# Optimization experiments

Measured on AMD Instinct MI355X. Metric: run time of the kernel, lower is better.

Reference implementation:

```python
import jax, jax.numpy as jnp
import numpy as np

BLOCK = 128          # per-block quantization group size (BLOCK_SIZE in source)
FP8_MAX = 448.0      # max representable magnitude of float8_e4m3fn


def _quantize(x2d):
    # Per-128-element block quantization along the last (contiguous) dim,
    # matching quantize_fp8_triton applied to the row-major flattened tensor.
    R, K = x2d.shape
    xb = x2d.reshape(R, K // BLOCK, BLOCK)
    s = jnp.max(jnp.abs(xb), axis=-1) / FP8_MAX            # [R, K//BLOCK] fp32 scales
    y = (xb / s[..., None]).astype(jnp.float8_e4m3fn)      # fp8 payload
    return y, s


def _dequantize(y, s):
    # Inline dequant: fp8 -> fp32 times per-block scale (fused into GEMM accum in the kernel).
    return (y.astype(jnp.float32) * s[..., None]).reshape(y.shape[0], -1)


def setup_inputs() -> dict:
    key = jax.random.key(0)
    kx, kw = jax.random.split(key)
    B, T, D, O = 4, 2048, 4096, 4096
    x = jax.random.normal(kx, (B, T, D), dtype=jnp.float32)
    limit = float(np.sqrt(6.0 / (D + O)))  # xavier_uniform_
    weight = jax.random.uniform(kw, (O, D), minval=-limit, maxval=limit, dtype=jnp.float32)
    return {"x": x, "weight": weight}


def reference(x, weight):
    B, T, D = x.shape
    xf = x.reshape(-1, D)                  # [M, K]
    xq, xs = _quantize(xf)                 # fp8 activations + per-(row,kblock) scales
    wq, ws = _quantize(weight)             # fp8 weights + per-(row,kblock) scales
    # Block-scaled GEMM: sum_i (A_i @ B_i^T) * a_s[:, i] * b_s[:, i]
    # expressed equivalently as dequant-then-matmul (identical math, fp32 accumulate).
    out = _dequantize(xq, xs) @ _dequantize(wq, ws).T      # [M, N]
    return out.reshape(B, T, -1)
```

## Files before the change

### kernel.cpp

```cpp
#include <hip/hip_runtime.h>

using u16 = unsigned short;
typedef int i32x4 __attribute__((ext_vector_type(4)));
typedef int i32x8 __attribute__((ext_vector_type(8)));
typedef float f32x4 __attribute__((ext_vector_type(4)));
typedef float f32x2 __attribute__((ext_vector_type(2)));
typedef float f32x16 __attribute__((ext_vector_type(16)));

#define SC1 0x7F7F7F7F

__device__ inline void async16(const void* g, void* l) {
    __builtin_amdgcn_global_load_lds(
        (__attribute__((address_space(1))) void*)(g),
        (__attribute__((address_space(3))) void*)(l),
        16, 0, 0);
}

__device__ inline i32x8 mk8(i32x4 lo, i32x4 hi) {
    return __builtin_shufflevector(lo, hi, 0, 1, 2, 3, 4, 5, 6, 7);
}

__global__ void quant_kernel(const float* __restrict__ in,
                             u16* __restrict__ outq,
                             float* __restrict__ outs,
                             long R) {
    long wid = (long)blockIdx.x * 4 + (threadIdx.x >> 6);
    int lane = threadIdx.x & 63;
    if (wid >= R * 32) return;

    float2 v = reinterpret_cast<const float2*>(in + wid * 128)[lane];
    float a = fmaxf(fabsf(v.x), fabsf(v.y));
#pragma unroll
    for (int off = 32; off; off >>= 1) a = fmaxf(a, __shfl_xor(a, off));

    float s = a / 448.0f;
    float qx = v.x / s;
    float qy = v.y / s;
    qx = fminf(fmaxf(qx, -448.0f), 448.0f);
    qy = fminf(fmaxf(qy, -448.0f), 448.0f);

    int pk = __builtin_amdgcn_cvt_pk_fp8_f32(qx, qy, 0, false);
    outq[wid * 64 + lane] = (u16)(pk & 0xFFFF);

    if (lane == 0) {
        long row = wid >> 5, kb = wid & 31;
        outs[kb * R + row] = s;
    }
}


#define SWZ(x) ((x) ^ ((((x) >> 7) & 7) << 4))

__global__ __launch_bounds__(512, 2) void gemm_fp8(
    const char* __restrict__ Aq, const char* __restrict__ Bq,
    const float* __restrict__ AscaleG, const float* __restrict__ BscaleG,
    float* __restrict__ C, int M, int N) {
    extern __shared__ __align__(16) char smem[];
    const int KB = 4096;

    const int tid = threadIdx.x;
    const int wid = tid >> 6;
    const int lane = tid & 63;
    const int l31 = lane & 31;
    const int lh = lane >> 5;
    const int wr = wid >> 2;
    const int wc = wid & 3;

    int nwg = gridDim.x, bid = blockIdx.x, swz = bid;
    if ((nwg & 7) == 0) swz = (bid & 7) * (nwg >> 3) + (bid >> 3);
    const int nbn = N >> 8;
    const long brow = (long)(swz / nbn) << 8;
    const long bcol = (long)(swz % nbn) << 8;

    const char* Abase = Aq + brow * KB;
    const char* Bbase = Bq + bcol * KB;

    int aofs[4];
#pragma unroll
    for (int c = 0; c < 4; ++c) {
        int dloc = c * 8192 + wid * 1024 + lane * 16;
        int l = SWZ(dloc);
        aofs[c] = (l >> 7) * KB + (l & 127);
    }

    int cox[4];
#pragma unroll
    for (int kh = 0; kh < 2; ++kh)
#pragma unroll
        for (int hh = 0; hh < 2; ++hh)
            cox[kh * 2 + hh] = (((kh << 6) | (lh << 5) | (hh << 4)) ^ ((lane & 7) << 4));

    int arowb[4], brown[2];
#pragma unroll
    for (int b = 0; b < 4; ++b) arowb[b] = (wr * 128 + b * 32 + l31) << 7;
#pragma unroll
    for (int n = 0; n < 2; ++n) brown[n] = (wc * 64 + n * 32 + l31) << 7;

#define STAGE(kb_, bufb) { \
    _Pragma("unroll") for (int c_ = 0; c_ < 4; ++c_) { \
        char* dA_ = smem + (bufb) * 32768 + c_ * 8192 + wid * 1024; \
        char* dB_ = dA_ + 65536; \
        async16(Abase + aofs[c_] + (kb_) * 128, dA_); \
        async16(Bbase + aofs[c_] + (kb_) * 128, dB_); } \
    if (wid == 0) \
        async16((const char*)AscaleG + ((long)(kb_) * M + brow) * 4 + lane * 16, \
                smem + 131072 + (bufb) * 1024); \
    if (wid == 1) \
        async16((const char*)BscaleG + ((long)(kb_) * N + bcol) * 4 + lane * 16, \
                smem + 133120 + (bufb) * 1024); }

    f32x16 acc[4][2];
#pragma unroll
    for (int b = 0; b < 4; ++b)
#pragma unroll
        for (int n = 0; n < 2; ++n)
#pragma unroll
            for (int e = 0; e < 16; ++e) acc[b][n][e] = 0.f;

    STAGE(0, 0);
    asm volatile("s_waitcnt vmcnt(0)" ::: "memory");
    __builtin_amdgcn_s_barrier();

    for (int kb = 0; kb < 32; ++kb) {
        const int buf = kb & 1;
        if (kb < 31) STAGE(kb + 1, buf ^ 1);

        const char* Ab = smem + buf * 32768;
        const char* Bb = Ab + 65536;
        const float* SaB = (const float*)(smem + 131072 + buf * 1024);
        const float* SbB = (const float*)(smem + 133120 + buf * 1024);

        i32x8 b8[2][2];
#pragma unroll
        for (int n = 0; n < 2; ++n)
#pragma unroll
            for (int kh = 0; kh < 2; ++kh)
                b8[n][kh] = mk8(*(const i32x4*)(Bb + brown[n] + cox[kh * 2]),
                                *(const i32x4*)(Bb + brown[n] + cox[kh * 2 + 1]));
        float sbv[2];
#pragma unroll
        for (int n = 0; n < 2; ++n) sbv[n] = SbB[wc * 64 + n * 32 + l31];

        __builtin_amdgcn_s_setprio(1);
#pragma unroll
        for (int b = 0; b < 4; ++b) {
            i32x8 a0 = mk8(*(const i32x4*)(Ab + arowb[b] + cox[0]),
                           *(const i32x4*)(Ab + arowb[b] + cox[1]));
            i32x8 a1 = mk8(*(const i32x4*)(Ab + arowb[b] + cox[2]),
                           *(const i32x4*)(Ab + arowb[b] + cox[3]));
            f32x4 sa4[4];
#pragma unroll
            for (int i = 0; i < 4; ++i)
                sa4[i] = *(const f32x4*)(SaB + wr * 128 + b * 32 + 4 * lh + 8 * i);
#pragma unroll
            for (int n = 0; n < 2; ++n) {
                f32x16 t = __builtin_amdgcn_mfma_scale_f32_32x32x64_f8f6f4(
                    a0, b8[n][0], (f32x16)(0.f), 0, 0, 0, SC1, 0, SC1);
                t = __builtin_amdgcn_mfma_scale_f32_32x32x64_f8f6f4(
                    a1, b8[n][1], t, 0, 0, 0, SC1, 0, SC1);
#pragma unroll
                for (int e = 0; e < 16; ++e)
                    acc[b][n][e] = fmaf(t[e], sa4[e >> 2][e & 3] * sbv[n],
                                        acc[b][n][e]);
            }
        }
        __builtin_amdgcn_s_setprio(0);

        asm volatile("s_waitcnt vmcnt(0)" ::: "memory");
        __builtin_amdgcn_s_barrier();
    }

#pragma unroll
    for (int b = 0; b < 4; ++b)
#pragma unroll
        for (int n = 0; n < 2; ++n)
#pragma unroll
            for (int e = 0; e < 16; ++e) {
                long r = brow + wr * 128 + b * 32 + (e & 3) + 8 * (e >> 2) + 4 * lh;
                long cc = bcol + wc * 64 + n * 32 + l31;
                C[r * (long)N + cc] = acc[b][n][e];
            }
#undef STAGE
}

extern "C" void kernel_launch(void* const* d_in, const int* in_sizes, int n_in,
                              void* d_out, int out_size, void* d_ws, size_t ws_size,
                              hipStream_t stream) {
    const float* x = (const float*)d_in[0];
    const float* w = (const float*)d_in[1];
    float* out = (float*)d_out;

    const int K = 4096;
    const long M = (long)in_sizes[0] / K;
    const long N = (long)in_sizes[1] / K;

    u16* Aq = (u16*)d_ws;
    u16* Bq = Aq + (size_t)M * K / 2;
    float* Asc = (float*)(Bq + (size_t)N * K / 2);
    float* Bsc = Asc + 32 * (size_t)M;

    const long nblkA = M * 32, nblkB = N * 32;
    quant_kernel<<<dim3((unsigned)((nblkA + 3) / 4)), dim3(256), 0, stream>>>(
        x, Aq, Asc, M);
    quant_kernel<<<dim3((unsigned)((nblkB + 3) / 4)), dim3(256), 0, stream>>>(
        w, Bq, Bsc, N);

    static int smem_set = 0;
    if (!smem_set) {
        hipFuncSetAttribute((const void*)gemm_fp8,
                            hipFuncAttributeMaxDynamicSharedMemorySize, 135168);
        smem_set = 1;
    }
    dim3 grid((unsigned)((M / 256) * (N / 256)));
    gemm_fp8<<<grid, dim3(512), 135168, stream>>>(
        (const char*)Aq, (const char*)Bq, Asc, Bsc, out, (int)M, (int)N);
}
```

Measured before the change: 289.7 us.

## Software-pipeline FP8 GEMM main loop with register double-buffered A bands

Restructures the K loop of the block-scaled FP8 GEMM into four phases per K block. The next A band is read from LDS while the current band runs MFMAs, and the global-to-LDS copies for the next K block are split across the phases. Scale loads are now issued by every wave instead of only waves 0 and 1, and the final K block is peeled off. The aim is to hide LDS read latency and spread global load issue more evenly across compute, at the cost of more barriers per iteration, redundant scale traffic and more register pressure.

Result: slower. 642.6 us (+121.8%).

```diff
diff --git a/kernel.cpp b/kernel.cpp
--- a/kernel.cpp
+++ b/kernel.cpp
@@ -51,12 +51,16 @@
 
 #define SWZ(x) ((x) ^ ((((x) >> 7) & 7) << 4))
 
+#define FENCE asm volatile("" ::: "memory");
+#define BARRIER { __builtin_amdgcn_s_barrier(); FENCE }
+#define VMC0 { asm volatile("s_waitcnt vmcnt(0)" ::: "memory"); }
+
 __global__ __launch_bounds__(512, 2) void gemm_fp8(
     const char* __restrict__ Aq, const char* __restrict__ Bq,
     const float* __restrict__ AscaleG, const float* __restrict__ BscaleG,
     float* __restrict__ C, int M, int N) {
     extern __shared__ __align__(16) char smem[];
-    const int KB = 4096;
+    const int KBYTES = 4096;
 
     const int tid = threadIdx.x;
     const int wid = tid >> 6;
@@ -72,15 +76,15 @@
     const long brow = (long)(swz / nbn) << 8;
     const long bcol = (long)(swz % nbn) << 8;
 
-    const char* Abase = Aq + brow * KB;
-    const char* Bbase = Bq + bcol * KB;
+    const char* Abase = Aq + brow * KBYTES;
+    const char* Bbase = Bq + bcol * KBYTES;
 
     int aofs[4];
 #pragma unroll
     for (int c = 0; c < 4; ++c) {
         int dloc = c * 8192 + wid * 1024 + lane * 16;
         int l = SWZ(dloc);
-        aofs[c] = (l >> 7) * KB + (l & 127);
+        aofs[c] = (l >> 7) * KBYTES + (l & 127);
     }
 
     int cox[4];
@@ -88,7 +92,8 @@
     for (int kh = 0; kh < 2; ++kh)
 #pragma unroll
         for (int hh = 0; hh < 2; ++hh)
-            cox[kh * 2 + hh] = (((kh << 6) | (lh << 5) | (hh << 4)) ^ ((lane & 7) << 4));
+            cox[kh * 2 + hh] =
+                (((kh << 6) | (lh << 5) | (hh << 4)) ^ ((lane & 7) << 4));
 
     int arowb[4], brown[2];
 #pragma unroll
@@ -96,18 +101,54 @@
 #pragma unroll
     for (int n = 0; n < 2; ++n) brown[n] = (wc * 64 + n * 32 + l31) << 7;
 
-#define STAGE(kb_, bufb) { \
-    _Pragma("unroll") for (int c_ = 0; c_ < 4; ++c_) { \
-        char* dA_ = smem + (bufb) * 32768 + c_ * 8192 + wid * 1024; \
-        char* dB_ = dA_ + 65536; \
-        async16(Abase + aofs[c_] + (kb_) * 128, dA_); \
-        async16(Bbase + aofs[c_] + (kb_) * 128, dB_); } \
-    if (wid == 0) \
-        async16((const char*)AscaleG + ((long)(kb_) * M + brow) * 4 + lane * 16, \
-                smem + 131072 + (bufb) * 1024); \
-    if (wid == 1) \
-        async16((const char*)BscaleG + ((long)(kb_) * N + bcol) * 4 + lane * 16, \
-                smem + 133120 + (bufb) * 1024); }
+#define STG_SCALES(kb1) { \
+    async16((const char*)AscaleG + ((long)(kb1) * M + brow) * 4 + lane * 16, \
+            smem + 131072 + ((kb1) & 1) * 1024); \
+    async16((const char*)BscaleG + ((long)(kb1) * N + bcol) * 4 + lane * 16, \
+            smem + 133120 + ((kb1) & 1) * 1024); }
+
+#define STG_DATA(kb1, c_) { \
+    char* dA_ = smem + ((kb1) & 1) * 32768 + (c_) * 8192 + wid * 1024; \
+    async16(Abase + aofs[c_] + (long)(kb1) * 128, dA_); \
+    async16(Bbase + aofs[c_] + (long)(kb1) * 128, dA_ + 65536); }
+
+#define RD_HEAD(bufb) { \
+    const char* Bb_ = smem + 65536 + (bufb) * 32768; \
+    _Pragma("unroll") for (int n_ = 0; n_ < 2; ++n_) \
+    _Pragma("unroll") for (int kh_ = 0; kh_ < 2; ++kh_) \
+        b8[n_][kh_] = mk8(*(const i32x4*)(Bb_ + brown[n_] + cox[kh_ * 2]), \
+                          *(const i32x4*)(Bb_ + brown[n_] + cox[kh_ * 2 + 1])); \
+    const float* Sb_ = (const float*)(smem + 133120 + (bufb) * 1024); \
+    sbv0 = Sb_[wc * 64 + l31]; \
+    sbv1 = Sb_[wc * 64 + 32 + l31]; }
+
+#define RD_BAND(b_, bufb, A0, A1, SA) { \
+    const char* Ab_ = smem + (bufb) * 32768; \
+    A0 = mk8(*(const i32x4*)(Ab_ + arowb[b_] + cox[0]), \
+             *(const i32x4*)(Ab_ + arowb[b_] + cox[1])); \
+    A1 = mk8(*(const i32x4*)(Ab_ + arowb[b_] + cox[2]), \
+             *(const i32x4*)(Ab_ + arowb[b_] + cox[3])); \
+    const float* Sa_ = (const float*)(smem + 131072 + (bufb) * 1024); \
+    _Pragma("unroll") for (int i_ = 0; i_ < 4; ++i_) \
+        SA[i_] = *(const f32x4*)(Sa_ + wr * 128 + (b_) * 32 + 4 * lh + 8 * i_); }
+
+#define COMPUTE(b_, A0, A1, SA) { \
+    __builtin_amdgcn_s_setprio(1); \
+    f32x16 t0_ = __builtin_amdgcn_mfma_scale_f32_32x32x64_f8f6f4( \
+        A0, b8[0][0], (f32x16)(0.f), 0, 0, 0, SC1, 0, SC1); \
+    t0_ = __builtin_amdgcn_mfma_scale_f32_32x32x64_f8f6f4( \
+        A1, b8[0][1], t0_, 0, 0, 0, SC1, 0, SC1); \
+    f32x16 t1_ = __builtin_amdgcn_mfma_scale_f32_32x32x64_f8f6f4( \
+        A0, b8[1][0], (f32x16)(0.f), 0, 0, 0, SC1, 0, SC1); \
+    t1_ = __builtin_amdgcn_mfma_scale_f32_32x32x64_f8f6f4( \
+        A1, b8[1][1], t1_, 0, 0, 0, SC1, 0, SC1); \
+    __builtin_amdgcn_s_setprio(0); \
+    _Pragma("unroll") for (int i_ = 0; i_ < 4; ++i_) \
+    _Pragma("unroll") for (int j_ = 0; j_ < 4; ++j_) { \
+        acc[b_][0][i_ * 4 + j_] = fmaf(t0_[i_ * 4 + j_], SA[i_][j_] * sbv0, \
+                                       acc[b_][0][i_ * 4 + j_]); \
+        acc[b_][1][i_ * 4 + j_] = fmaf(t1_[i_ * 4 + j_], SA[i_][j_] * sbv1, \
+                                       acc[b_][1][i_ * 4 + j_]); } }
 
     f32x16 acc[4][2];
 #pragma unroll
@@ -117,57 +158,45 @@
 #pragma unroll
             for (int e = 0; e < 16; ++e) acc[b][n][e] = 0.f;
 
-    STAGE(0, 0);
-    asm volatile("s_waitcnt vmcnt(0)" ::: "memory");
-    __builtin_amdgcn_s_barrier();
-
-    for (int kb = 0; kb < 32; ++kb) {
-        const int buf = kb & 1;
-        if (kb < 31) STAGE(kb + 1, buf ^ 1);
-
-        const char* Ab = smem + buf * 32768;
-        const char* Bb = Ab + 65536;
-        const float* SaB = (const float*)(smem + 131072 + buf * 1024);
-        const float* SbB = (const float*)(smem + 133120 + buf * 1024);
-
-        i32x8 b8[2][2];
-#pragma unroll
-        for (int n = 0; n < 2; ++n)
-#pragma unroll
-            for (int kh = 0; kh < 2; ++kh)
-                b8[n][kh] = mk8(*(const i32x4*)(Bb + brown[n] + cox[kh * 2]),
-                                *(const i32x4*)(Bb + brown[n] + cox[kh * 2 + 1]));
-        float sbv[2];
-#pragma unroll
-        for (int n = 0; n < 2; ++n) sbv[n] = SbB[wc * 64 + n * 32 + l31];
-
-        __builtin_amdgcn_s_setprio(1);
-#pragma unroll
-        for (int b = 0; b < 4; ++b) {
-            i32x8 a0 = mk8(*(const i32x4*)(Ab + arowb[b] + cox[0]),
-                           *(const i32x4*)(Ab + arowb[b] + cox[1]));
-            i32x8 a1 = mk8(*(const i32x4*)(Ab + arowb[b] + cox[2]),
-                           *(const i32x4*)(Ab + arowb[b] + cox[3]));
-            f32x4 sa4[4];
-#pragma unroll
-            for (int i = 0; i < 4; ++i)
-                sa4[i] = *(const f32x4*)(SaB + wr * 128 + b * 32 + 4 * lh + 8 * i);
-#pragma unroll
-            for (int n = 0; n < 2; ++n) {
-                f32x16 t = __builtin_amdgcn_mfma_scale_f32_32x32x64_f8f6f4(
-                    a0, b8[n][0], (f32x16)(0.f), 0, 0, 0, SC1, 0, SC1);
-                t = __builtin_amdgcn_mfma_scale_f32_32x32x64_f8f6f4(
-                    a1, b8[n][1], t, 0, 0, 0, SC1, 0, SC1);
-#pragma unroll
-                for (int e = 0; e < 16; ++e)
-                    acc[b][n][e] = fmaf(t[e], sa4[e >> 2][e & 3] * sbv[n],
-                                        acc[b][n][e]);
-            }
-        }
-        __builtin_amdgcn_s_setprio(0);
-
-        asm volatile("s_waitcnt vmcnt(0)" ::: "memory");
-        __builtin_amdgcn_s_barrier();
+    i32x8 b8[2][2];
+    i32x8 a0_0, a1_0, a0_1, a1_1;
+    f32x4 saA[4], saB[4];
+    float sbv0, sbv1;
+
+    STG_SCALES(0);
+    STG_DATA(0, 0); STG_DATA(0, 1); STG_DATA(0, 2); STG_DATA(0, 3);
+    VMC0; BARRIER;
+    RD_BAND(0, 0, a0_0, a1_0, saA);
+
+    for (int kb = 0; kb < 31; ++kb) {
+        const int bufb = kb & 1;
+        RD_HEAD(bufb);
+        STG_SCALES(kb + 1);
+        STG_DATA(kb + 1, 0); STG_DATA(kb + 1, 1);
+        RD_BAND(1, bufb, a0_1, a1_1, saB);
+        COMPUTE(0, a0_0, a1_0, saA);
+        BARRIER;
+        STG_DATA(kb + 1, 2); STG_DATA(kb + 1, 3);
+        RD_BAND(2, bufb, a0_0, a1_0, saA);
+        COMPUTE(1, a0_1, a1_1, saB);
+        BARRIER;
+        RD_BAND(3, bufb, a0_1, a1_1, saB);
+        COMPUTE(2, a0_0, a1_0, saA);
+        BARRIER;
+        VMC0; BARRIER;
+        RD_BAND(0, bufb ^ 1, a0_0, a1_0, saA);
+        COMPUTE(3, a0_1, a1_1, saB);
+        BARRIER;
+    }
+    {
+        RD_HEAD(1);
+        RD_BAND(1, 1, a0_1, a1_1, saB);
+        COMPUTE(0, a0_0, a1_0, saA);
+        RD_BAND(2, 1, a0_0, a1_0, saA);
+        COMPUTE(1, a0_1, a1_1, saB);
+        RD_BAND(3, 1, a0_1, a1_1, saB);
+        COMPUTE(2, a0_0, a1_0, saA);
+        COMPUTE(3, a0_1, a1_1, saB);
     }
 
 #pragma unroll
@@ -180,7 +209,11 @@
                 long cc = bcol + wc * 64 + n * 32 + l31;
                 C[r * (long)N + cc] = acc[b][n][e];
             }
-#undef STAGE
+#undef STG_SCALES
+#undef STG_DATA
+#undef RD_HEAD
+#undef RD_BAND
+#undef COMPUTE
 }
 
 extern "C" void kernel_launch(void* const* d_in, const int* in_sizes, int n_in,
```
